# Kernel optimization log

Measured on AMD Instinct MI355X. Metric: run time of the kernel, lower is better.

Reference implementation:

```python
import jax, jax.numpy as jnp
import numpy as np

H, VS, VT, S, T = 512, 32000, 32000, 256, 256
EPS = 1e-12


def _normalize(x):
    # torch.nn.functional.normalize over last dim, p=2, eps=1e-12
    n = jnp.sqrt(jnp.sum(x * x, axis=-1, keepdims=True))
    return x / jnp.maximum(n, EPS)


def setup_inputs() -> dict:
    key = jax.random.key(0)
    ks = jax.random.split(key, 16)
    std = 0.01
    return {
        'src_nums': jax.random.randint(ks[0], (S,), 0, VS, dtype=jnp.int32),
        'tgt_nums': jax.random.randint(ks[1], (T,), 0, VT, dtype=jnp.int32),
        'enc_emb_W': std * jax.random.normal(ks[2], (VS, H), jnp.float32),
        'enc_h0': std * jax.random.normal(ks[3], (H,), jnp.float32),
        'enc_W_hi': std * jax.random.normal(ks[4], (H, H), jnp.float32),
        'enc_W_hh': std * jax.random.normal(ks[5], (H, H), jnp.float32),
        'enc_b': std * jax.random.normal(ks[6], (H,), jnp.float32),
        'dec_emb_W': std * jax.random.normal(ks[7], (VT, H), jnp.float32),
        'dec_h0': std * jax.random.normal(ks[8], (H,), jnp.float32),
        'dec_W_hi': std * jax.random.normal(ks[9], (H, H), jnp.float32),
        'dec_W_hh': std * jax.random.normal(ks[10], (H, H), jnp.float32),
        'dec_b': std * jax.random.normal(ks[11], (H,), jnp.float32),
        'tnh_W': std * jax.random.normal(ks[12], (H, 2 * H), jnp.float32),
        'tnh_b': std * jax.random.normal(ks[13], (H,), jnp.float32),
        'out_W': std * jax.random.normal(ks[14], (VT, H), jnp.float32),
    }


def reference(src_nums, tgt_nums, enc_emb_W, enc_h0, enc_W_hi, enc_W_hh, enc_b,
              dec_emb_W, dec_h0, dec_W_hi, dec_W_hh, dec_b, tnh_W, tnh_b, out_W):
    # ---- Encoder: embed + normalize, then sequential RNN ----
    src_emb = _normalize(enc_emb_W[src_nums])  # [S, H]

    def enc_step(h, e):
        h2 = jnp.tanh(enc_W_hi @ e + enc_W_hh @ h + enc_b)
        return h2, h2

    _, hs = jax.lax.scan(enc_step, enc_h0, src_emb)
    h_seq = jnp.concatenate([enc_h0[None, :], hs], axis=0)  # [S+1, H]

    # ---- Decoder: per-step attention + output + teacher-forced input ----
    def dec_step(h, t):
        # Bahdanau-style dot attention over encoder states
        weights = jax.nn.softmax(h_seq @ h)        # [S+1]
        c = weights @ h_seq                         # [H]
        z = jnp.tanh(tnh_W @ jnp.concatenate([c, h]) + tnh_b)  # [H]
        logp = jax.nn.log_softmax(out_W @ z)        # [VT]
        nll = -logp[t]
        e = _normalize(dec_emb_W[t])                # [H]
        h2 = jnp.tanh(dec_W_hi @ e + dec_W_hh @ h + dec_b)
        return h2, nll

    _, nlls = jax.lax.scan(dec_step, dec_h0, tgt_nums)
    return jnp.mean(nlls)
```

## Files before the change

### kernel.cpp

```cpp
#include <hip/hip_runtime.h>

typedef _Float16 f16;
typedef _Float16 f16x2 __attribute__((ext_vector_type(2)));
typedef _Float16 half8 __attribute__((ext_vector_type(8)));
typedef float f32x4 __attribute__((ext_vector_type(4)));

#define Hh 512
#define TT 256
#define VTOT 32000
#define S4H 100.0f

__device__ inline int dot8i4(int a, int b, int c) {
#if __has_builtin(__builtin_amdgcn_sdot8)
    return __builtin_amdgcn_sdot8(a, b, c, false);
#else
    int s = c;
#pragma unroll
    for (int i = 0; i < 8; ++i)
        s += ((a << (28 - 4 * i)) >> 28) * ((b << (28 - 4 * i)) >> 28);
    return s;
#endif
}

__device__ inline float tanh_fast(float x) {
    float ax = fabsf(x);
    float t = __expf(-2.f * ax);
    float th = (1.f - t) * __builtin_amdgcn_rcpf(1.f + t);
    return copysignf(th, x);
}

__device__ inline float block_sum(float v, float* red) {
#pragma unroll
    for (int o = 1; o < 64; o <<= 1) v += __shfl_xor(v, o);
    if ((threadIdx.x & 63) == 0) red[threadIdx.x >> 6] = v;
    __syncthreads();
    v = red[0] + red[1] + red[2] + red[3];
    __syncthreads();
    return v;
}

__device__ inline float block_max(float v, float* red) {
#pragma unroll
    for (int o = 1; o < 64; o <<= 1) v = fmaxf(v, __shfl_xor(v, o));
    if ((threadIdx.x & 63) == 0) red[threadIdx.x >> 6] = v;
    __syncthreads();
    v = fmaxf(fmaxf(red[0], red[1]), fmaxf(red[2], red[3]));
    __syncthreads();
    return v;
}

__global__ void __launch_bounds__(256) k_prep(
    const int* __restrict__ src, const int* __restrict__ tgt,
    const float* __restrict__ encW, const float* __restrict__ decW,
    const float* __restrict__ eh0, const float* __restrict__ dh0,
    const float* __restrict__ encWhh, const float* __restrict__ decWhh,
    f16* __restrict__ embH, float* __restrict__ h_seq, float* __restrict__ Hd,
    unsigned int* __restrict__ Wq, float* __restrict__ sWf) {
    const int b = blockIdx.x, tid = threadIdx.x;
    if (b >= 514) {
        const int bc = b - 514;
        const int R = bc * 4 + (tid >> 6);
        const int c = R >> 9, r = R & 511, j = tid & 63;
        const float* s = (c ? decWhh : encWhh) + (size_t)r * Hh + j * 8;
        float4 v0 = ((const float4*)s)[0];
        float4 v1 = ((const float4*)s)[1];
        float vv[8] = {v0.x, v0.y, v0.z, v0.w, v1.x, v1.y, v1.z, v1.w};
        float m = 0.f;
#pragma unroll
        for (int k = 0; k < 8; ++k) m = fmaxf(m, fabsf(vv[k]));
#pragma unroll
        for (int o = 1; o < 64; o <<= 1) m = fmaxf(m, __shfl_xor(m, o));
        m = fmaxf(m, 1e-30f);
        float qs = 7.f / m;
        unsigned int dw = 0;
#pragma unroll
        for (int k = 0; k < 8; ++k) {
            int q = (int)rintf(vv[k] * qs);
            dw |= ((unsigned int)(q & 0xF)) << (4 * k);
        }
        const int u = j >> 2, dwi = j & 3;
        Wq[((((size_t)(c * 16 + u)) * 512 + r) << 2) + dwi] = dw;
        if (j == 0) sWf[c * 512 + r] = m * (1.f / (7.f * S4H));
        return;
    }
    if (b >= 512) {
        const int c = b - 512;
        float2 v = ((const float2*)(c ? dh0 : eh0))[tid];
        if (c == 0)
            ((float2*)h_seq)[tid] = v;
        else
            ((float2*)Hd)[tid] = v;
        return;
    }
    const int c = b >> 8, t = b & 255;
    const int idx = c ? tgt[t] : src[t];
    const float* row = (c ? decW : encW) + (size_t)idx * Hh;
    float2 v = ((const float2*)row)[tid];
    __shared__ float red[4];
    float tot = block_sum(v.x * v.x + v.y * v.y, red);
    float inv = 1.f / fmaxf(sqrtf(tot), 1e-12f);
    f16* orow = embH + ((size_t)c * TT + t) * Hh;
    f16x2 o = {(f16)(v.x * inv), (f16)(v.y * inv)};
    ((f16x2*)orow)[tid] = o;
}

__global__ void __launch_bounds__(256) k_pgemm(const f16* __restrict__ embH,
                                               const float* __restrict__ eWhi,
                                               const float* __restrict__ eb,
                                               const float* __restrict__ dWhi,
                                               const float* __restrict__ db,
                                               float* __restrict__ P) {
    const int c = blockIdx.y;
    const int v0 = blockIdx.x * 64, tid = threadIdx.x;
    const float* Wv = c ? dWhi : eWhi;
    const float* bias = c ? db : eb;
    const f16* Zb = embH + (size_t)c * TT * Hh;
    const int w = tid >> 6, l = tid & 63;
    const int l15 = l & 15, l4 = l >> 4;
    __shared__ __align__(16) f16 Wt[64][136];
    __shared__ __align__(16) f16 Zt[256][136];

    f32x4 acc[16];
#pragma unroll
    for (int tt = 0; tt < 16; ++tt) acc[tt] = (f32x4){0.f, 0.f, 0.f, 0.f};

    for (int kc = 0; kc < 4; ++kc) {
        const int k0 = kc * 128;
#pragma unroll
        for (int p = 0; p < 8; ++p) {
            int g = p * 256 + tid;
            int row = g >> 5, f4 = g & 31;
            float4 v = *((const float4*)(Wv + (size_t)(v0 + row) * Hh + k0 + f4 * 4));
            f16x2 lo = {(f16)v.x, (f16)v.y};
            f16x2 hi = {(f16)v.z, (f16)v.w};
            uint2 u;
            u.x = __builtin_bit_cast(unsigned, lo);
            u.y = __builtin_bit_cast(unsigned, hi);
            *((uint2*)&Wt[row][f4 * 4]) = u;
        }
#pragma unroll
        for (int p = 0; p < 16; ++p) {
            int g = p * 256 + tid;
            int row = g >> 4, u = g & 15;
            *((uint4*)&Zt[row][u * 8]) =
                *((const uint4*)(Zb + (size_t)row * Hh + k0 + u * 8));
        }
        __syncthreads();
        half8 a[4];
#pragma unroll
        for (int ks = 0; ks < 4; ++ks)
            a[ks] = *((const half8*)&Wt[w * 16 + l15][ks * 32 + l4 * 8]);
#pragma unroll
        for (int tt = 0; tt < 16; ++tt) {
#pragma unroll
            for (int ks = 0; ks < 4; ++ks) {
                half8 b = *((const half8*)&Zt[tt * 16 + l15][ks * 32 + l4 * 8]);
                acc[tt] = __builtin_amdgcn_mfma_f32_16x16x32_f16(a[ks], b, acc[tt],
                                                                 0, 0, 0);
            }
        }
        __syncthreads();
    }
    const int ibase = v0 + w * 16 + l4 * 4;
    float b0 = bias[ibase], b1 = bias[ibase + 1];
    float b2 = bias[ibase + 2], b3 = bias[ibase + 3];
#pragma unroll
    for (int tt = 0; tt < 16; ++tt) {
        int t = tt * 16 + l15;
        float4 st;
        st.x = acc[tt][0] + b0;
        st.y = acc[tt][1] + b1;
        st.z = acc[tt][2] + b2;
        st.w = acc[tt][3] + b3;
        *((float4*)(P + ((size_t)c * TT + t) * Hh + ibase)) = st;
    }
}

__global__ void __launch_bounds__(512, 2) k_chain(
    const uint4* __restrict__ Wq, const float* __restrict__ sWf,
    const float* __restrict__ P, const float* __restrict__ eh0,
    const float* __restrict__ dh0, float* __restrict__ h_seq,
    float* __restrict__ Hd) {
    const int c = blockIdx.x, t = threadIdx.x;
    __shared__ __align__(16) int hq[2][64];

    uint4 wq[16];
#pragma unroll
    for (int u = 0; u < 16; ++u) wq[u] = Wq[(size_t)(c * 16 + u) * 512 + t];
#pragma unroll
    for (int u = 0; u < 16; ++u)
        asm volatile("" : "+v"(wq[u].x), "+v"(wq[u].y), "+v"(wq[u].z),
                          "+v"(wq[u].w));
    const float frow = sWf[c * 512 + t];

    {
        float hv = (c ? dh0 : eh0)[t];
        int q = (int)rintf(fminf(fmaxf(hv * S4H, -7.f), 7.f));
        int b1 = (q & 0xF) | ((__shfl_down(q, 1) & 0xF) << 4);
        int b2 = (b1 & 0xFF) | ((__shfl_down(b1, 2) & 0xFF) << 8);
        int b4 = (b2 & 0xFFFF) | (__shfl_down(b2, 4) << 16);
        if ((t & 7) == 0) hq[0][t >> 3] = b4;
    }
    __syncthreads();

    const float* Pc = P + (size_t)c * TT * Hh;
    float pv = Pc[t];

    for (int step = 0; step < 256; ++step) {
        float pvn;
        if (step < 255) pvn = Pc[(size_t)(step + 1) * Hh + t];
        const uint4* hp = (const uint4*)hq[step & 1];
        int a0 = 0, a1 = 0;
#pragma unroll
        for (int u = 0; u < 16; ++u) {
            uint4 hv = hp[u];
            uint4 w0 = wq[u];
            a0 = dot8i4((int)w0.x, (int)hv.x, a0);
            a1 = dot8i4((int)w0.y, (int)hv.y, a1);
            a0 = dot8i4((int)w0.z, (int)hv.z, a0);
            a1 = dot8i4((int)w0.w, (int)hv.w, a1);
        }
        float hnew = tanh_fast((float)(a0 + a1) * frow + pv);
        pv = pvn;
        if (c == 0)
            h_seq[(size_t)(step + 1) * Hh + t] = hnew;
        else if (step < 255)
            Hd[(size_t)(step + 1) * Hh + t] = hnew;
        int q = (int)rintf(fminf(fmaxf(hnew * S4H, -7.f), 7.f));
        int b1 = (q & 0xF) | ((__shfl_down(q, 1) & 0xF) << 4);
        int b2 = (b1 & 0xFF) | ((__shfl_down(b1, 2) & 0xFF) << 8);
        int b4 = (b2 & 0xFFFF) | (__shfl_down(b2, 4) << 16);
        if ((t & 7) == 0) hq[(step + 1) & 1][t >> 3] = b4;
        asm volatile("s_waitcnt lgkmcnt(0)\ns_barrier" ::: "memory");
    }
}

__global__ void __launch_bounds__(256) k_scores(const float* __restrict__ h_seq,
                                                const float* __restrict__ Hd,
                                                float* __restrict__ CH) {
    const int t0 = blockIdx.x * 2, tid = threadIdx.x;
    __shared__ float h0s[Hh], h1s[Hh];
    __shared__ float w0[257], w1[257];
    __shared__ float red[4];
    ((float2*)h0s)[tid] = ((const float2*)(Hd + (size_t)t0 * Hh))[tid];
    ((float2*)h1s)[tid] = ((const float2*)(Hd + (size_t)(t0 + 1) * Hh))[tid];
    __syncthreads();
    float a0 = 0.f, a1 = 0.f;
    {
        const float4* row = (const float4*)(h_seq + (size_t)tid * Hh);
        for (int j = 0; j < Hh / 4; ++j) {
            float4 v = row[j];
            a0 += v.x * h0s[4 * j] + v.y * h0s[4 * j + 1] + v.z * h0s[4 * j + 2] +
                  v.w * h0s[4 * j + 3];
            a1 += v.x * h1s[4 * j] + v.y * h1s[4 * j + 1] + v.z * h1s[4 * j + 2] +
                  v.w * h1s[4 * j + 3];
        }
    }
    float sb0 = -3.0e38f, sb1 = -3.0e38f;
    if (tid == 0) {
        const float4* row = (const float4*)(h_seq + (size_t)256 * Hh);
        float x0 = 0.f, x1 = 0.f;
        for (int j = 0; j < Hh / 4; ++j) {
            float4 v = row[j];
            x0 += v.x * h0s[4 * j] + v.y * h0s[4 * j + 1] + v.z * h0s[4 * j + 2] +
                  v.w * h0s[4 * j + 3];
            x1 += v.x * h1s[4 * j] + v.y * h1s[4 * j + 1] + v.z * h1s[4 * j + 2] +
                  v.w * h1s[4 * j + 3];
        }
        sb0 = x0;
        sb1 = x1;
    }
    float m0 = block_max(fmaxf(a0, sb0), red);
    float e0 = expf(a0 - m0);
    float ee0 = (tid == 0) ? expf(sb0 - m0) : 0.f;
    float tot0 = block_sum(e0 + ee0, red);
    float inv0 = 1.f / tot0;
    w0[tid] = e0 * inv0;
    if (tid == 0) w0[256] = ee0 * inv0;
    float m1 = block_max(fmaxf(a1, sb1), red);
    float e1 = expf(a1 - m1);
    float ee1 = (tid == 0) ? expf(sb1 - m1) : 0.f;
    float tot1 = block_sum(e1 + ee1, red);
    float inv1 = 1.f / tot1;
    w1[tid] = e1 * inv1;
    if (tid == 0) w1[256] = ee1 * inv1;
    __syncthreads();
    const float2* hs2 = (const float2*)h_seq;
    float2 c0 = {0.f, 0.f}, c1 = {0.f, 0.f};
    for (int s = 0; s < 257; ++s) {
        float2 v = hs2[(size_t)s * 256 + tid];
        float W0 = w0[s], W1 = w1[s];
        c0.x += W0 * v.x;
        c0.y += W0 * v.y;
        c1.x += W1 * v.x;
        c1.y += W1 * v.y;
    }
    float* ch0 = CH + (size_t)t0 * (2 * Hh);
    float* ch1 = CH + (size_t)(t0 + 1) * (2 * Hh);
    ((float2*)ch0)[tid] = c0;
    ((float2*)ch1)[tid] = c1;
    ((float2*)(ch0 + Hh))[tid] = ((float2*)h0s)[tid];
    ((float2*)(ch1 + Hh))[tid] = ((float2*)h1s)[tid];
}

__global__ void __launch_bounds__(256) k_zgemm(const float* __restrict__ CH,
                                               const float* __restrict__ tnhW,
                                               const float* __restrict__ tnhb,
                                               f16* __restrict__ Zh) {
    const int t0 = blockIdx.x * 8, tid = threadIdx.x;
    const int i = tid + blockIdx.y * 256;
    __shared__ __align__(16) float chs[8][2 * Hh];
#pragma unroll
    for (int rr = 0; rr < 8; ++rr) {
        ((float4*)chs[rr])[tid] =
            ((const float4*)(CH + (size_t)(t0 + rr) * 2 * Hh))[tid];
    }
    __syncthreads();
    const float4* wp = (const float4*)(tnhW + (size_t)i * 2 * Hh);
    float acc[8] = {0.f, 0.f, 0.f, 0.f, 0.f, 0.f, 0.f, 0.f};
    for (int j = 0; j < 2 * Hh / 4; ++j) {
        float4 w0 = wp[j];
#pragma unroll
        for (int rr = 0; rr < 8; ++rr) {
            float4 e = ((const float4*)chs[rr])[j];
            acc[rr] += w0.x * e.x + w0.y * e.y + w0.z * e.z + w0.w * e.w;
        }
    }
    float b0 = tnhb[i];
#pragma unroll
    for (int rr = 0; rr < 8; ++rr)
        Zh[(size_t)(t0 + rr) * Hh + i] = (f16)tanhf(acc[rr] + b0);
}

__global__ void __launch_bounds__(256) k_logits(const f16* __restrict__ Zh,
                                                const float* __restrict__ outW,
                                                const int* __restrict__ tgt,
                                                float* __restrict__ denom,
                                                float* __restrict__ ltgt) {
    const int v0 = blockIdx.x * 64, tid = threadIdx.x;
    const int w = tid >> 6, l = tid & 63;
    const int l15 = l & 15, l4 = l >> 4;
    __shared__ __align__(16) f16 Wt[64][136];
    __shared__ __align__(16) f16 Zt[256][136];
    __shared__ float tsum[4][256];
    __shared__ int tgs[256];
    if (tid < 256) tgs[tid] = tgt[tid];

    f32x4 acc[16];
#pragma unroll
    for (int tt = 0; tt < 16; ++tt) acc[tt] = (f32x4){0.f, 0.f, 0.f, 0.f};

    for (int kc = 0; kc < 4; ++kc) {
        const int k0 = kc * 128;
#pragma unroll
        for (int p = 0; p < 8; ++p) {
            int g = p * 256 + tid;
            int row = g >> 5, f4 = g & 31;
            float4 v = *((const float4*)(outW + (size_t)(v0 + row) * Hh + k0 + f4 * 4));
            f16x2 lo = {(f16)v.x, (f16)v.y};
            f16x2 hi = {(f16)v.z, (f16)v.w};
            uint2 u;
            u.x = __builtin_bit_cast(unsigned, lo);
            u.y = __builtin_bit_cast(unsigned, hi);
            *((uint2*)&Wt[row][f4 * 4]) = u;
        }
#pragma unroll
        for (int p = 0; p < 16; ++p) {
            int g = p * 256 + tid;
            int row = g >> 4, u = g & 15;
            *((uint4*)&Zt[row][u * 8]) =
                *((const uint4*)(Zh + (size_t)row * Hh + k0 + u * 8));
        }
        __syncthreads();
        half8 a[4];
#pragma unroll
        for (int ks = 0; ks < 4; ++ks)
            a[ks] = *((const half8*)&Wt[w * 16 + l15][ks * 32 + l4 * 8]);
#pragma unroll
        for (int tt = 0; tt < 16; ++tt) {
#pragma unroll
            for (int ks = 0; ks < 4; ++ks) {
                half8 b = *((const half8*)&Zt[tt * 16 + l15][ks * 32 + l4 * 8]);
                acc[tt] = __builtin_amdgcn_mfma_f32_16x16x32_f16(a[ks], b, acc[tt],
                                                                 0, 0, 0);
            }
        }
        __syncthreads();
    }
    const int vbase = v0 + w * 16 + l4 * 4;
#pragma unroll
    for (int tt = 0; tt < 16; ++tt) {
        float e = __expf(acc[tt][0]) + __expf(acc[tt][1]) + __expf(acc[tt][2]) +
                  __expf(acc[tt][3]);
        e += __shfl_xor(e, 16);
        e += __shfl_xor(e, 32);
        if (l4 == 0) tsum[w][tt * 16 + l15] = e;
        int tglob = tt * 16 + l15;
        int rel = tgs[tglob] - vbase;
        if (rel >= 0 && rel < 4) {
            float val = (rel == 0) ? acc[tt][0]
                        : (rel == 1) ? acc[tt][1]
                        : (rel == 2) ? acc[tt][2]
                                     : acc[tt][3];
            ltgt[tglob] = val;
        }
    }
    __syncthreads();
    if (tid < 256) {
        float s = tsum[0][tid] + tsum[1][tid] + tsum[2][tid] + tsum[3][tid];
        atomicAdd(&denom[tid], s);
    }
}

__global__ void k_final(const float* __restrict__ denom, const float* __restrict__ ltgt,
                        float* __restrict__ out) {
    const int t = threadIdx.x;
    float nll = logf(denom[t]) - ltgt[t];
    __shared__ float red[4];
    float v = nll;
#pragma unroll
    for (int o = 1; o < 64; o <<= 1) v += __shfl_xor(v, o);
    if ((t & 63) == 0) red[t >> 6] = v;
    __syncthreads();
    if (t == 0) out[0] = (red[0] + red[1] + red[2] + red[3]) * (1.f / 256.f);
}

extern "C" void kernel_launch(void* const* d_in, const int* in_sizes, int n_in,
                              void* d_out, int out_size, void* d_ws, size_t ws_size,
                              hipStream_t stream) {
    (void)in_sizes; (void)n_in; (void)out_size; (void)ws_size;
    const int* src = (const int*)d_in[0];
    const int* tgt = (const int*)d_in[1];
    const float* enc_emb = (const float*)d_in[2];
    const float* enc_h0 = (const float*)d_in[3];
    const float* enc_Whi = (const float*)d_in[4];
    const float* enc_Whh = (const float*)d_in[5];
    const float* enc_b = (const float*)d_in[6];
    const float* dec_emb = (const float*)d_in[7];
    const float* dec_h0 = (const float*)d_in[8];
    const float* dec_Whi = (const float*)d_in[9];
    const float* dec_Whh = (const float*)d_in[10];
    const float* dec_b = (const float*)d_in[11];
    const float* tnhW = (const float*)d_in[12];
    const float* tnhb = (const float*)d_in[13];
    const float* outW = (const float*)d_in[14];
    float* out = (float*)d_out;
    char* ws = (char*)d_ws;

    float* denom = (float*)ws;
    float* ltgt = (float*)(ws + 1024);
    size_t off = 4096;
    f16* embH = (f16*)(ws + off);       off += (size_t)2 * TT * Hh * 4;
    float* P = (float*)(ws + off);      off += (size_t)2 * TT * Hh * 4;
    float* h_seq = (float*)(ws + off);  off += (size_t)264 * Hh * 4;
    float* Hd = (float*)(ws + off);     off += (size_t)256 * Hh * 4;
    float* CH = (float*)(ws + off);     off += (size_t)TT * 2 * Hh * 4;
    f16* Zh = (f16*)(ws + off);         off += (size_t)TT * Hh * 2;
    uint4* Wq = (uint4*)(ws + off);     off += (size_t)2 * Hh * Hh;
    float* sWf = (float*)(ws + off);    off += (size_t)2 * Hh * 4;

    hipMemsetAsync(ws, 0, 4096, stream);
    k_prep<<<770, 256, 0, stream>>>(src, tgt, enc_emb, dec_emb, enc_h0, dec_h0,
                                    enc_Whh, dec_Whh, embH, h_seq, Hd,
                                    (unsigned int*)Wq, sWf);
    k_pgemm<<<dim3(8, 2), 256, 0, stream>>>(embH, enc_Whi, enc_b, dec_Whi, dec_b, P);
    k_chain<<<2, 512, 0, stream>>>(Wq, sWf, P, enc_h0, dec_h0, h_seq, Hd);
    k_scores<<<128, 256, 0, stream>>>(h_seq, Hd, CH);
    k_zgemm<<<dim3(32, 2), 256, 0, stream>>>(CH, tnhW, tnhb, Zh);
    k_logits<<<500, 256, 0, stream>>>(Zh, outW, tgt, denom, ltgt);
    k_final<<<1, 256, 0, stream>>>(denom, ltgt, out);
}
```

Measured before the change: 317.9 us.

## Overlap fp16 weight conversion with serial RNN chain and fuse front kernels

Extra blocks are added to the latency-bound two-block recurrence kernel. While the chain runs, they convert out_W and tnh_W to fp16 in workspace, so the logits and tanh GEMMs later load half the bytes and skip the per-tile conversion. The embedding gather and normalize are fused into the input-projection GEMM, which removes the prep and pgemm split. The tanh layer becomes an MFMA GEMM over fp16 context and hidden inputs. The new path depends on the workspace being large enough, and the conversion blocks compete with the chain for memory bandwidth.

```diff
diff --git a/kernel.cpp b/kernel.cpp
--- a/kernel.cpp
+++ b/kernel.cpp
@@ -9,6 +9,8 @@
 #define TT 256
 #define VTOT 32000
 #define S4H 100.0f
+#define NO_ELEMS 16384000L
+#define NT_ELEMS 524288L
 
 __device__ inline int dot8i4(int a, int b, int c) {
 #if __has_builtin(__builtin_amdgcn_sdot8)
@@ -49,16 +51,27 @@
     return v;
 }
 
-__global__ void __launch_bounds__(256) k_prep(
+__global__ void __launch_bounds__(256) k_front(
     const int* __restrict__ src, const int* __restrict__ tgt,
     const float* __restrict__ encW, const float* __restrict__ decW,
     const float* __restrict__ eh0, const float* __restrict__ dh0,
     const float* __restrict__ encWhh, const float* __restrict__ decWhh,
-    f16* __restrict__ embH, float* __restrict__ h_seq, float* __restrict__ Hd,
+    const float* __restrict__ eWhi, const float* __restrict__ eb,
+    const float* __restrict__ dWhi, const float* __restrict__ db,
+    float* __restrict__ P, float* __restrict__ h_seq, float* __restrict__ Hd,
     unsigned int* __restrict__ Wq, float* __restrict__ sWf) {
     const int b = blockIdx.x, tid = threadIdx.x;
-    if (b >= 514) {
-        const int bc = b - 514;
+    if (b >= 272) {
+        const int c = b - 272;
+        float2 v = ((const float2*)(c ? dh0 : eh0))[tid];
+        if (c == 0)
+            ((float2*)h_seq)[tid] = v;
+        else
+            ((float2*)Hd)[tid] = v;
+        return;
+    }
+    if (b >= 16) {
+        const int bc = b - 16;
         const int R = bc * 4 + (tid >> 6);
         const int c = R >> 9, r = R & 511, j = tid & 63;
         const float* s = (c ? decWhh : encWhh) + (size_t)r * Hh + j * 8;
@@ -83,42 +96,29 @@
         if (j == 0) sWf[c * 512 + r] = m * (1.f / (7.f * S4H));
         return;
     }
-    if (b >= 512) {
-        const int c = b - 512;
-        float2 v = ((const float2*)(c ? dh0 : eh0))[tid];
-        if (c == 0)
-            ((float2*)h_seq)[tid] = v;
-        else
-            ((float2*)Hd)[tid] = v;
-        return;
-    }
-    const int c = b >> 8, t = b & 255;
-    const int idx = c ? tgt[t] : src[t];
-    const float* row = (c ? decW : encW) + (size_t)idx * Hh;
-    float2 v = ((const float2*)row)[tid];
-    __shared__ float red[4];
-    float tot = block_sum(v.x * v.x + v.y * v.y, red);
-    float inv = 1.f / fmaxf(sqrtf(tot), 1e-12f);
-    f16* orow = embH + ((size_t)c * TT + t) * Hh;
-    f16x2 o = {(f16)(v.x * inv), (f16)(v.y * inv)};
-    ((f16x2*)orow)[tid] = o;
-}
-
-__global__ void __launch_bounds__(256) k_pgemm(const f16* __restrict__ embH,
-                                               const float* __restrict__ eWhi,
-                                               const float* __restrict__ eb,
-                                               const float* __restrict__ dWhi,
-                                               const float* __restrict__ db,
-                                               float* __restrict__ P) {
-    const int c = blockIdx.y;
-    const int v0 = blockIdx.x * 64, tid = threadIdx.x;
+    const int c = b >> 3;
+    const int v0 = (b & 7) * 64;
     const float* Wv = c ? dWhi : eWhi;
     const float* bias = c ? db : eb;
-    const f16* Zb = embH + (size_t)c * TT * Hh;
+    const float* Etab = c ? decW : encW;
     const int w = tid >> 6, l = tid & 63;
     const int l15 = l & 15, l4 = l >> 4;
     __shared__ __align__(16) f16 Wt[64][136];
     __shared__ __align__(16) f16 Zt[256][136];
+    __shared__ float norms[256];
+    __shared__ int idxs[256];
+    idxs[tid] = c ? tgt[tid] : src[tid];
+    __syncthreads();
+    {
+        const float4* er = (const float4*)(Etab + (size_t)idxs[tid] * Hh);
+        float s = 0.f;
+        for (int j = 0; j < Hh / 4; ++j) {
+            float4 v = er[j];
+            s += v.x * v.x + v.y * v.y + v.z * v.z + v.w * v.w;
+        }
+        norms[tid] = 1.f / fmaxf(sqrtf(s), 1e-12f);
+    }
+    __syncthreads();
 
     f32x4 acc[16];
 #pragma unroll
@@ -142,8 +142,20 @@
         for (int p = 0; p < 16; ++p) {
             int g = p * 256 + tid;
             int row = g >> 4, u = g & 15;
-            *((uint4*)&Zt[row][u * 8]) =
-                *((const uint4*)(Zb + (size_t)row * Hh + k0 + u * 8));
+            const float* rs = Etab + (size_t)idxs[row] * Hh + k0 + u * 8;
+            float4 a0 = ((const float4*)rs)[0];
+            float4 a1 = ((const float4*)rs)[1];
+            float nm = norms[row];
+            f16x2 p0 = {(f16)(a0.x * nm), (f16)(a0.y * nm)};
+            f16x2 p1 = {(f16)(a0.z * nm), (f16)(a0.w * nm)};
+            f16x2 p2 = {(f16)(a1.x * nm), (f16)(a1.y * nm)};
+            f16x2 p3 = {(f16)(a1.z * nm), (f16)(a1.w * nm)};
+            uint4 uu;
+            uu.x = __builtin_bit_cast(unsigned, p0);
+            uu.y = __builtin_bit_cast(unsigned, p1);
+            uu.z = __builtin_bit_cast(unsigned, p2);
+            uu.w = __builtin_bit_cast(unsigned, p3);
+            *((uint4*)&Zt[row][u * 8]) = uu;
         }
         __syncthreads();
         half8 a[4];
@@ -154,8 +166,8 @@
         for (int tt = 0; tt < 16; ++tt) {
 #pragma unroll
             for (int ks = 0; ks < 4; ++ks) {
-                half8 b = *((const half8*)&Zt[tt * 16 + l15][ks * 32 + l4 * 8]);
-                acc[tt] = __builtin_amdgcn_mfma_f32_16x16x32_f16(a[ks], b, acc[tt],
+                half8 bb = *((const half8*)&Zt[tt * 16 + l15][ks * 32 + l4 * 8]);
+                acc[tt] = __builtin_amdgcn_mfma_f32_16x16x32_f16(a[ks], bb, acc[tt],
                                                                  0, 0, 0);
             }
         }
@@ -180,8 +192,40 @@
     const uint4* __restrict__ Wq, const float* __restrict__ sWf,
     const float* __restrict__ P, const float* __restrict__ eh0,
     const float* __restrict__ dh0, float* __restrict__ h_seq,
-    float* __restrict__ Hd) {
+    float* __restrict__ Hd, const float* __restrict__ outW,
+    const float* __restrict__ tnhW, f16* __restrict__ outWh,
+    f16* __restrict__ tnhWh) {
     const int c = blockIdx.x, t = threadIdx.x;
+    if (c >= 2) {
+        const long nthreads = (long)(gridDim.x - 2) * 512;
+        long g = (long)(c - 2) * 512 + t;
+        const long N8 = (NO_ELEMS + NT_ELEMS) / 8;
+        for (; g < N8; g += nthreads) {
+            long e = g * 8;
+            const float* s;
+            f16* d;
+            if (e < NO_ELEMS) {
+                s = outW + e;
+                d = outWh + e;
+            } else {
+                s = tnhW + (e - NO_ELEMS);
+                d = tnhWh + (e - NO_ELEMS);
+            }
+            float4 v0 = ((const float4*)s)[0];
+            float4 v1 = ((const float4*)s)[1];
+            f16x2 p0 = {(f16)v0.x, (f16)v0.y};
+            f16x2 p1 = {(f16)v0.z, (f16)v0.w};
+            f16x2 p2 = {(f16)v1.x, (f16)v1.y};
+            f16x2 p3 = {(f16)v1.z, (f16)v1.w};
+            uint4 u;
+            u.x = __builtin_bit_cast(unsigned, p0);
+            u.y = __builtin_bit_cast(unsigned, p1);
+            u.z = __builtin_bit_cast(unsigned, p2);
+            u.w = __builtin_bit_cast(unsigned, p3);
+            *((uint4*)d) = u;
+        }
+        return;
+    }
     __shared__ __align__(16) int hq[2][64];
 
     uint4 wq[16];
@@ -237,7 +281,7 @@
 
 __global__ void __launch_bounds__(256) k_scores(const float* __restrict__ h_seq,
                                                 const float* __restrict__ Hd,
-                                                float* __restrict__ CH) {
+                                                f16* __restrict__ CHh) {
     const int t0 = blockIdx.x * 2, tid = threadIdx.x;
     __shared__ float h0s[Hh], h1s[Hh];
     __shared__ float w0[257], w1[257];
@@ -295,45 +339,103 @@
         c1.x += W1 * v.x;
         c1.y += W1 * v.y;
     }
-    float* ch0 = CH + (size_t)t0 * (2 * Hh);
-    float* ch1 = CH + (size_t)(t0 + 1) * (2 * Hh);
-    ((float2*)ch0)[tid] = c0;
-    ((float2*)ch1)[tid] = c1;
-    ((float2*)(ch0 + Hh))[tid] = ((float2*)h0s)[tid];
-    ((float2*)(ch1 + Hh))[tid] = ((float2*)h1s)[tid];
-}
-
-__global__ void __launch_bounds__(256) k_zgemm(const float* __restrict__ CH,
+    f16* ch0 = CHh + (size_t)t0 * (2 * Hh);
+    f16* ch1 = CHh + (size_t)(t0 + 1) * (2 * Hh);
+    f16x2 o0 = {(f16)c0.x, (f16)c0.y};
+    f16x2 o1 = {(f16)c1.x, (f16)c1.y};
+    ((f16x2*)ch0)[tid] = o0;
+    ((f16x2*)ch1)[tid] = o1;
+    float2 hh0 = ((float2*)h0s)[tid];
+    float2 hh1 = ((float2*)h1s)[tid];
+    f16x2 ho0 = {(f16)hh0.x, (f16)hh0.y};
+    f16x2 ho1 = {(f16)hh1.x, (f16)hh1.y};
+    ((f16x2*)(ch0 + Hh))[tid] = ho0;
+    ((f16x2*)(ch1 + Hh))[tid] = ho1;
+}
+
+template <bool W16>
+__global__ void __launch_bounds__(256) k_zmfma(const f16* __restrict__ CHh,
                                                const float* __restrict__ tnhW,
+                                               const f16* __restrict__ tnhWh,
                                                const float* __restrict__ tnhb,
                                                f16* __restrict__ Zh) {
-    const int t0 = blockIdx.x * 8, tid = threadIdx.x;
-    const int i = tid + blockIdx.y * 256;
-    __shared__ __align__(16) float chs[8][2 * Hh];
-#pragma unroll
-    for (int rr = 0; rr < 8; ++rr) {
-        ((float4*)chs[rr])[tid] =
-            ((const float4*)(CH + (size_t)(t0 + rr) * 2 * Hh))[tid];
-    }
-    __syncthreads();
-    const float4* wp = (const float4*)(tnhW + (size_t)i * 2 * Hh);
-    float acc[8] = {0.f, 0.f, 0.f, 0.f, 0.f, 0.f, 0.f, 0.f};
-    for (int j = 0; j < 2 * Hh / 4; ++j) {
-        float4 w0 = wp[j];
-#pragma unroll
-        for (int rr = 0; rr < 8; ++rr) {
-            float4 e = ((const float4*)chs[rr])[j];
-            acc[rr] += w0.x * e.x + w0.y * e.y + w0.z * e.z + w0.w * e.w;
-        }
-    }
-    float b0 = tnhb[i];
-#pragma unroll
-    for (int rr = 0; rr < 8; ++rr)
-        Zh[(size_t)(t0 + rr) * Hh + i] = (f16)tanhf(acc[rr] + b0);
-}
-
+    const int v0 = blockIdx.x * 64, t0 = blockIdx.y * 128, tid = threadIdx.x;
+    const int w = tid >> 6, l = tid & 63;
+    const int l15 = l & 15, l4 = l >> 4;
+    __shared__ __align__(16) f16 Wt[64][136];
+    __shared__ __align__(16) f16 Zt[128][136];
+
+    f32x4 acc[8];
+#pragma unroll
+    for (int tt = 0; tt < 8; ++tt) acc[tt] = (f32x4){0.f, 0.f, 0.f, 0.f};
+
+    for (int kc = 0; kc < 8; ++kc) {
+        const int k0 = kc * 128;
+        if constexpr (W16) {
+#pragma unroll
+            for (int p = 0; p < 4; ++p) {
+                int g = p * 256 + tid;
+                int row = g >> 4, u = g & 15;
+                *((uint4*)&Wt[row][u * 8]) =
+                    *((const uint4*)(tnhWh + (size_t)(v0 + row) * 1024 + k0 + u * 8));
+            }
+        } else {
+#pragma unroll
+            for (int p = 0; p < 8; ++p) {
+                int g = p * 256 + tid;
+                int row = g >> 5, f4 = g & 31;
+                float4 v =
+                    *((const float4*)(tnhW + (size_t)(v0 + row) * 1024 + k0 + f4 * 4));
+                f16x2 lo = {(f16)v.x, (f16)v.y};
+                f16x2 hi = {(f16)v.z, (f16)v.w};
+                uint2 u;
+                u.x = __builtin_bit_cast(unsigned, lo);
+                u.y = __builtin_bit_cast(unsigned, hi);
+                *((uint2*)&Wt[row][f4 * 4]) = u;
+            }
+        }
+#pragma unroll
+        for (int p = 0; p < 8; ++p) {
+            int g = p * 256 + tid;
+            int row = g >> 4, u = g & 15;
+            *((uint4*)&Zt[row][u * 8]) =
+                *((const uint4*)(CHh + (size_t)(t0 + row) * 1024 + k0 + u * 8));
+        }
+        __syncthreads();
+        half8 a[4];
+#pragma unroll
+        for (int ks = 0; ks < 4; ++ks)
+            a[ks] = *((const half8*)&Wt[w * 16 + l15][ks * 32 + l4 * 8]);
+#pragma unroll
+        for (int tt = 0; tt < 8; ++tt) {
+#pragma unroll
+            for (int ks = 0; ks < 4; ++ks) {
+                half8 bb = *((const half8*)&Zt[tt * 16 + l15][ks * 32 + l4 * 8]);
+                acc[tt] = __builtin_amdgcn_mfma_f32_16x16x32_f16(a[ks], bb, acc[tt],
+                                                                 0, 0, 0);
+            }
+        }
+        __syncthreads();
+    }
+    const int ibase = v0 + w * 16 + l4 * 4;
+    float b0 = tnhb[ibase], b1 = tnhb[ibase + 1];
+    float b2 = tnhb[ibase + 2], b3 = tnhb[ibase + 3];
+#pragma unroll
+    for (int tt = 0; tt < 8; ++tt) {
+        int t = t0 + tt * 16 + l15;
+        f16x2 lo = {(f16)tanhf(acc[tt][0] + b0), (f16)tanhf(acc[tt][1] + b1)};
+        f16x2 hi = {(f16)tanhf(acc[tt][2] + b2), (f16)tanhf(acc[tt][3] + b3)};
+        uint2 u;
+        u.x = __builtin_bit_cast(unsigned, lo);
+        u.y = __builtin_bit_cast(unsigned, hi);
+        *((uint2*)(Zh + (size_t)t * Hh + ibase)) = u;
+    }
+}
+
+template <bool W16>
 __global__ void __launch_bounds__(256) k_logits(const f16* __restrict__ Zh,
                                                 const float* __restrict__ outW,
+                                                const f16* __restrict__ outWh,
                                                 const int* __restrict__ tgt,
                                                 float* __restrict__ denom,
                                                 float* __restrict__ ltgt) {
@@ -352,17 +454,28 @@
 
     for (int kc = 0; kc < 4; ++kc) {
         const int k0 = kc * 128;
-#pragma unroll
-        for (int p = 0; p < 8; ++p) {
-            int g = p * 256 + tid;
-            int row = g >> 5, f4 = g & 31;
-            float4 v = *((const float4*)(outW + (size_t)(v0 + row) * Hh + k0 + f4 * 4));
-            f16x2 lo = {(f16)v.x, (f16)v.y};
-            f16x2 hi = {(f16)v.z, (f16)v.w};
-            uint2 u;
-            u.x = __builtin_bit_cast(unsigned, lo);
-            u.y = __builtin_bit_cast(unsigned, hi);
-            *((uint2*)&Wt[row][f4 * 4]) = u;
+        if constexpr (W16) {
+#pragma unroll
+            for (int p = 0; p < 4; ++p) {
+                int g = p * 256 + tid;
+                int row = g >> 4, u = g & 15;
+                *((uint4*)&Wt[row][u * 8]) =
+                    *((const uint4*)(outWh + (size_t)(v0 + row) * Hh + k0 + u * 8));
+            }
+        } else {
+#pragma unroll
+            for (int p = 0; p < 8; ++p) {
+                int g = p * 256 + tid;
+                int row = g >> 5, f4 = g & 31;
+                float4 v =
+                    *((const float4*)(outW + (size_t)(v0 + row) * Hh + k0 + f4 * 4));
+                f16x2 lo = {(f16)v.x, (f16)v.y};
+                f16x2 hi = {(f16)v.z, (f16)v.w};
+                uint2 u;
+                u.x = __builtin_bit_cast(unsigned, lo);
+                u.y = __builtin_bit_cast(unsigned, hi);
+                *((uint2*)&Wt[row][f4 * 4]) = u;
+            }
         }
 #pragma unroll
         for (int p = 0; p < 16; ++p) {
@@ -380,8 +493,8 @@
         for (int tt = 0; tt < 16; ++tt) {
 #pragma unroll
             for (int ks = 0; ks < 4; ++ks) {
-                half8 b = *((const half8*)&Zt[tt * 16 + l15][ks * 32 + l4 * 8]);
-                acc[tt] = __builtin_amdgcn_mfma_f32_16x16x32_f16(a[ks], b, acc[tt],
+                half8 bb = *((const half8*)&Zt[tt * 16 + l15][ks * 32 + l4 * 8]);
+                acc[tt] = __builtin_amdgcn_mfma_f32_16x16x32_f16(a[ks], bb, acc[tt],
                                                                  0, 0, 0);
             }
         }
@@ -428,7 +541,7 @@
 extern "C" void kernel_launch(void* const* d_in, const int* in_sizes, int n_in,
                               void* d_out, int out_size, void* d_ws, size_t ws_size,
                               hipStream_t stream) {
-    (void)in_sizes; (void)n_in; (void)out_size; (void)ws_size;
+    (void)in_sizes; (void)n_in; (void)out_size;
     const int* src = (const int*)d_in[0];
     const int* tgt = (const int*)d_in[1];
     const float* enc_emb = (const float*)d_in[2];
@@ -450,23 +563,35 @@
     float* denom = (float*)ws;
     float* ltgt = (float*)(ws + 1024);
     size_t off = 4096;
-    f16* embH = (f16*)(ws + off);       off += (size_t)2 * TT * Hh * 4;
     float* P = (float*)(ws + off);      off += (size_t)2 * TT * Hh * 4;
     float* h_seq = (float*)(ws + off);  off += (size_t)264 * Hh * 4;
     float* Hd = (float*)(ws + off);     off += (size_t)256 * Hh * 4;
-    float* CH = (float*)(ws + off);     off += (size_t)TT * 2 * Hh * 4;
+    f16* CHh = (f16*)(ws + off);        off += (size_t)TT * 2 * Hh * 2;
     f16* Zh = (f16*)(ws + off);         off += (size_t)TT * Hh * 2;
     uint4* Wq = (uint4*)(ws + off);     off += (size_t)2 * Hh * Hh;
     float* sWf = (float*)(ws + off);    off += (size_t)2 * Hh * 4;
+    f16* outWh = (f16*)(ws + off);      size_t off_big = off + NO_ELEMS * 2;
+    f16* tnhWh = (f16*)(ws + off_big);  off_big += NT_ELEMS * 2;
+    const bool big = ws_size >= off_big;
 
     hipMemsetAsync(ws, 0, 4096, stream);
-    k_prep<<<770, 256, 0, stream>>>(src, tgt, enc_emb, dec_emb, enc_h0, dec_h0,
-                                    enc_Whh, dec_Whh, embH, h_seq, Hd,
-                                    (unsigned int*)Wq, sWf);
-    k_pgemm<<<dim3(8, 2), 256, 0, stream>>>(embH, enc_Whi, enc_b, dec_Whi, dec_b, P);
-    k_chain<<<2, 512, 0, stream>>>(Wq, sWf, P, enc_h0, dec_h0, h_seq, Hd);
-    k_scores<<<128, 256, 0, stream>>>(h_seq, Hd, CH);
-    k_zgemm<<<dim3(32, 2), 256, 0, stream>>>(CH, tnhW, tnhb, Zh);
-    k_logits<<<500, 256, 0, stream>>>(Zh, outW, tgt, denom, ltgt);
+    k_front<<<274, 256, 0, stream>>>(src, tgt, enc_emb, dec_emb, enc_h0, dec_h0,
+                                     enc_Whh, dec_Whh, enc_Whi, enc_b, dec_Whi,
+                                     dec_b, P, h_seq, Hd, (unsigned int*)Wq, sWf);
+    if (big) {
+        k_chain<<<128, 512, 0, stream>>>(Wq, sWf, P, enc_h0, dec_h0, h_seq, Hd,
+                                         outW, tnhW, outWh, tnhWh);
+    } else {
+        k_chain<<<2, 512, 0, stream>>>(Wq, sWf, P, enc_h0, dec_h0, h_seq, Hd,
+                                       outW, tnhW, outWh, tnhWh);
+    }
+    k_scores<<<128, 256, 0, stream>>>(h_seq, Hd, CHh);
+    if (big) {
+        k_zmfma<true><<<dim3(8, 2), 256, 0, stream>>>(CHh, tnhW, tnhWh, tnhb, Zh);
+        k_logits<true><<<500, 256, 0, stream>>>(Zh, outW, outWh, tgt, denom, ltgt);
+    } else {
+        k_zmfma<false><<<dim3(8, 2), 256, 0, stream>>>(CHh, tnhW, tnhWh, tnhb, Zh);
+        k_logits<false><<<500, 256, 0, stream>>>(Zh, outW, outWh, tgt, denom, ltgt);
+    }
     k_final<<<1, 256, 0, stream>>>(denom, ltgt, out);
 }
```

After: 311.4 us. 1.02x faster.
